# Optimization experiments

Hardware: AMD Instinct MI355X
Metric: run time of the kernel (lower is better)

## Reference

```python
import jax, jax.numpy as jnp
import numpy as np

TEMPERATURE = 0.5
COS_EPS = 1e-8  # torch.nn.CosineSimilarity default eps


def setup_inputs() -> dict:
    key = jax.random.key(0)
    k1, k2 = jax.random.split(key)
    N, D = 4096, 128
    z_i = jax.random.normal(k1, (N, D), dtype=jnp.float32)
    z_j = jax.random.normal(k2, (N, D), dtype=jnp.float32)
    return {"z_i": z_i, "z_j": z_j}


def reference(z_i, z_j):
    t = TEMPERATURE
    # L2-normalize each row (torch.norm over dim=1, then divide)
    zi = z_i / jnp.linalg.norm(z_i, axis=1, keepdims=True)
    zj = z_j / jnp.linalg.norm(z_j, axis=1, keepdims=True)
    z_ij = jnp.concatenate([zi, zj], axis=0)  # [2N, D]
    z_ji = jnp.concatenate([zj, zi], axis=0)  # [2N, D]
    # Full pairwise similarity matrix, scaled by temperature: [2N, 2N]
    sim = jnp.matmul(z_ij, z_ij.T) / t
    exp_sim = jnp.exp(sim)
    exp_sum = jnp.sum(exp_sim, axis=1)          # row reduction
    diag = jnp.diagonal(exp_sim)                # self-similarity terms
    # numerator: exp(cosine_similarity(z_ij, z_ji) / t) — positive pairs
    cos = jnp.sum(z_ij * z_ji, axis=1) / jnp.maximum(
        jnp.linalg.norm(z_ij, axis=1) * jnp.linalg.norm(z_ji, axis=1), COS_EPS)
    numerator = jnp.exp(cos / t)
    denominator = exp_sum - diag
    loss = -jnp.log(numerator / denominator)
    return jnp.mean(loss)
```

## Files before the change

### kernel.cpp

```cpp
#include <hip/hip_runtime.h>
#include <hip/hip_bf16.h>

typedef __attribute__((ext_vector_type(4))) int int4v;
typedef __attribute__((ext_vector_type(8))) int int8v;
typedef __attribute__((ext_vector_type(16))) float floatx16;

#define D_DIM 128
#define SCALE_F 1.6986436f
#define CS 16
#define CTILE 64
#define BLK_ROWS 256
#define MREP 2
#define UNIT_SCALE 0x7F7F7F7F

typedef __attribute__((address_space(1))) const unsigned int GUI;
typedef __attribute__((address_space(3))) unsigned int LUI;
#define GLOAD16(g, l) __builtin_amdgcn_global_load_lds((GUI*)(g), (LUI*)(l), 16, 0, 0)

__global__ void prep_kernel(const float* __restrict__ zi,
                            const float* __restrict__ zj,
                            unsigned char* __restrict__ Z8,
                            float* __restrict__ posdot,
                            float* __restrict__ selfarg, int N) {
    int r = blockIdx.x * 4 + (threadIdx.x >> 6);
    int t = threadIdx.x & 63;
    const float* pi = zi + (size_t)r * D_DIM;
    const float* pj = zj + (size_t)r * D_DIM;
    float a0 = pi[2 * t], a1 = pi[2 * t + 1];
    float b0 = pj[2 * t], b1 = pj[2 * t + 1];
    float ssi = a0*a0 + a1*a1;
    float ssj = b0*b0 + b1*b1;
    float sij = a0*b0 + a1*b1;
#pragma unroll
    for (int off = 1; off < 64; off <<= 1) {
        ssi += __shfl_xor(ssi, off);
        ssj += __shfl_xor(ssj, off);
        sij += __shfl_xor(sij, off);
    }
    float ni = sqrtf(ssi), nj = sqrtf(ssj);
    float ri = SCALE_F / ni, rj = SCALE_F / nj;
    int ui = __builtin_amdgcn_cvt_pk_fp8_f32(a0 * ri, a1 * ri, 0, false);
    int uj = __builtin_amdgcn_cvt_pk_fp8_f32(b0 * rj, b1 * rj, 0, false);
    *(ushort*)&Z8[(size_t)r * D_DIM + 2 * t]       = (ushort)(ui & 0xffff);
    *(ushort*)&Z8[(size_t)(r + N) * D_DIM + 2 * t] = (ushort)(uj & 0xffff);
    float fi0 = __builtin_amdgcn_cvt_f32_fp8(ui, 0);
    float fi1 = __builtin_amdgcn_cvt_f32_fp8(ui, 1);
    float fj0 = __builtin_amdgcn_cvt_f32_fp8(uj, 0);
    float fj1 = __builtin_amdgcn_cvt_f32_fp8(uj, 1);
    float sdi = fi0*fi0 + fi1*fi1;
    float sdj = fj0*fj0 + fj1*fj1;
#pragma unroll
    for (int off = 1; off < 64; off <<= 1) {
        sdi += __shfl_xor(sdi, off);
        sdj += __shfl_xor(sdj, off);
    }
    if (t == 0) {
        posdot[r] = sij / fmaxf(ni * nj, 1e-8f);
        selfarg[r]     = sdi;
        selfarg[r + N] = sdj;
    }
}

__global__ __launch_bounds__(512, 4)
void main_kernel(const unsigned char* __restrict__ Z8,
                 float* __restrict__ rowpart, int N2) {
    __shared__ unsigned char Btile[2][CTILE * D_DIM];

    const int tid  = threadIdx.x;
    const int lane = tid & 63;
    const int wave = tid >> 6;
    const int mw   = wave & 3;
    const int nh   = wave >> 2;
    const int c32  = lane & 31;
    const int h    = lane >> 5;
    const int rwave0 = blockIdx.x * BLK_ROWS + mw * 64;
    const int c0base = blockIdx.y * (N2 / CS);

    const int ntile = (N2 / CS) / CTILE;

    const int scol = tid >> 3;
    const int ssl  = (tid & 7) ^ (scol & 7);
    const unsigned char* gsrc = Z8 + (size_t)(c0base + scol) * D_DIM + ssl * 16;
    const size_t tadv = (size_t)CTILE * D_DIM;

    GLOAD16(gsrc, &Btile[0][(size_t)tid * 16]);

    int8v afrag[MREP][2];
#pragma unroll
    for (int rb = 0; rb < MREP; ++rb) {
        const unsigned char* ap = Z8 + (size_t)(rwave0 + rb * 32 + c32) * D_DIM + h * 32;
        afrag[rb][0] = *(const int8v*)(ap);
        afrag[rb][1] = *(const int8v*)(ap + 64);
    }
#pragma unroll
    for (int rb = 0; rb < MREP; ++rb) {
        asm volatile("" : "+v"(afrag[rb][0]));
        asm volatile("" : "+v"(afrag[rb][1]));
    }

    floatx16 rowacc[MREP];
#pragma unroll
    for (int rb = 0; rb < MREP; ++rb)
        rowacc[rb] = (floatx16)0.0f;

    __syncthreads();

    for (int t = 0; t < ntile; ++t) {
        if (t + 1 < ntile)
            GLOAD16(gsrc + (size_t)(t + 1) * tadv,
                    &Btile[(t + 1) & 1][(size_t)tid * 16]);

        const unsigned char* buf = Btile[t & 1];
        const int bcol = nh * 32 + c32;
        const int cb   = bcol * D_DIM;
        const int c7   = bcol & 7;
        int4v l00 = *(const int4v*)&buf[cb + (((h * 2 + 0) ^ c7) * 16)];
        int4v l01 = *(const int4v*)&buf[cb + (((h * 2 + 1) ^ c7) * 16)];
        int4v l10 = *(const int4v*)&buf[cb + (((4 + h * 2 + 0) ^ c7) * 16)];
        int4v l11 = *(const int4v*)&buf[cb + (((4 + h * 2 + 1) ^ c7) * 16)];
        int8v b0 = {l00[0], l00[1], l00[2], l00[3], l01[0], l01[1], l01[2], l01[3]};
        int8v b1 = {l10[0], l10[1], l10[2], l10[3], l11[0], l11[1], l11[2], l11[3]};

#pragma unroll
        for (int rb = 0; rb < MREP; ++rb) {
            floatx16 acc = (floatx16)0.0f;
            acc = __builtin_amdgcn_mfma_scale_f32_32x32x64_f8f6f4(
                      afrag[rb][0], b0, acc, 0, 0, 0, UNIT_SCALE, 0, UNIT_SCALE);
            acc = __builtin_amdgcn_mfma_scale_f32_32x32x64_f8f6f4(
                      afrag[rb][1], b1, acc, 0, 0, 0, UNIT_SCALE, 0, UNIT_SCALE);
#pragma unroll
            for (int g = 0; g < 16; ++g)
                rowacc[rb][g] += __builtin_amdgcn_exp2f(acc[g]);
        }
        __syncthreads();
    }

#pragma unroll
    for (int rb = 0; rb < MREP; ++rb)
#pragma unroll
        for (int g = 0; g < 16; ++g) {
            float v = rowacc[rb][g];
            v += __shfl_xor(v, 1);
            v += __shfl_xor(v, 2);
            v += __shfl_xor(v, 4);
            v += __shfl_xor(v, 8);
            v += __shfl_xor(v, 16);
            if (c32 == 0) {
                int grow = rwave0 + rb * 32 + (g & 3) + 8 * (g >> 2) + 4 * h;
                rowpart[(size_t)(blockIdx.y * 2 + nh) * N2 + grow] = v;
            }
        }
}

__global__ void finalize1_kernel(const float* __restrict__ rowpart,
                                 const float* __restrict__ selfarg,
                                 const float* __restrict__ posdot,
                                 float* __restrict__ bpart, int N2, int NP) {
    __shared__ float red[4];
    int tid = threadIdx.x;
    int r = blockIdx.x * 256 + tid;
    float d0 = 0.f, d1 = 0.f, d2 = 0.f, d3 = 0.f;
#pragma unroll
    for (int q = 0; q < 2 * CS; q += 4) {
        d0 += rowpart[(size_t)(q + 0) * N2 + r];
        d1 += rowpart[(size_t)(q + 1) * N2 + r];
        d2 += rowpart[(size_t)(q + 2) * N2 + r];
        d3 += rowpart[(size_t)(q + 3) * N2 + r];
    }
    float denom = (d0 + d1) + (d2 + d3);
    denom -= __builtin_amdgcn_exp2f(selfarg[r]);
    float pos = posdot[r < NP ? r : r - NP];
    float v = logf(denom) - 2.0f * pos;
#pragma unroll
    for (int off = 1; off < 64; off <<= 1) v += __shfl_xor(v, off);
    if ((tid & 63) == 0) red[tid >> 6] = v;
    __syncthreads();
    if (tid == 0) bpart[blockIdx.x] = red[0] + red[1] + red[2] + red[3];
}

__global__ void finalize2_kernel(const float* __restrict__ bpart,
                                 float* __restrict__ out, int nb, int N2) {
    int t = threadIdx.x;
    float v = (t < nb) ? bpart[t] : 0.0f;
#pragma unroll
    for (int off = 1; off < 64; off <<= 1) v += __shfl_xor(v, off);
    if (t == 0) out[0] = v / (float)N2;
}

extern "C" void kernel_launch(void* const* d_in, const int* in_sizes, int n_in,
                              void* d_out, int out_size, void* d_ws, size_t ws_size,
                              hipStream_t stream) {
    const float* zi = (const float*)d_in[0];
    const float* zj = (const float*)d_in[1];
    const int N  = in_sizes[0] / D_DIM;
    const int N2 = 2 * N;

    char* w = (char*)d_ws;
    unsigned char* Z8 = (unsigned char*)w;
    size_t off = (size_t)N2 * D_DIM;
    float* posdot  = (float*)(w + off);  off += (size_t)N  * sizeof(float);
    float* selfarg = (float*)(w + off);  off += (size_t)N2 * sizeof(float);
    float* rowpart = (float*)(w + off);  off += (size_t)(2 * CS) * N2 * sizeof(float);
    float* bpart   = (float*)(w + off);

    prep_kernel<<<N / 4, 256, 0, stream>>>(zi, zj, Z8, posdot, selfarg, N);
    dim3 grid(N2 / BLK_ROWS, CS);
    main_kernel<<<grid, 512, 0, stream>>>(Z8, rowpart, N2);
    const int nb = N2 / 256;
    finalize1_kernel<<<nb, 256, 0, stream>>>(rowpart, selfarg, posdot, bpart, N2, N);
    finalize2_kernel<<<1, 64, 0, stream>>>(bpart, (float*)d_out, nb, N2);
}
```

Before: 32.55 us.

## Fuse finalize kernels into main kernel via last-block atomic ticket

Removes the two finalize kernel launches. Each main_kernel block now increments a global ticket counter, and the last block to finish reduces all row partials and writes the mean loss. The ticket is reset inside prep_kernel. This saves two launch gaps, but the final reduction over 8192 rows x 32 partials now runs serially in a single 512-thread block, which may cost more than the launches it replaces.

```diff
diff --git a/kernel.cpp b/kernel.cpp
--- a/kernel.cpp
+++ b/kernel.cpp
@@ -12,6 +12,7 @@
 #define BLK_ROWS 256
 #define MREP 2
 #define UNIT_SCALE 0x7F7F7F7F
+#define NBLOCKS (32 * CS)
 
 typedef __attribute__((address_space(1))) const unsigned int GUI;
 typedef __attribute__((address_space(3))) unsigned int LUI;
@@ -21,7 +22,9 @@
                             const float* __restrict__ zj,
                             unsigned char* __restrict__ Z8,
                             float* __restrict__ posdot,
-                            float* __restrict__ selfarg, int N) {
+                            float* __restrict__ selfarg,
+                            int* __restrict__ ticket, int N) {
+    if (blockIdx.x == 0 && threadIdx.x == 0) *ticket = 0;
     int r = blockIdx.x * 4 + (threadIdx.x >> 6);
     int t = threadIdx.x & 63;
     const float* pi = zi + (size_t)r * D_DIM;
@@ -63,8 +66,14 @@
 
 __global__ __launch_bounds__(512, 4)
 void main_kernel(const unsigned char* __restrict__ Z8,
-                 float* __restrict__ rowpart, int N2) {
+                 float* __restrict__ rowpart,
+                 const float* __restrict__ selfarg,
+                 const float* __restrict__ posdot,
+                 int* __restrict__ ticket,
+                 float* __restrict__ out, int N2, int NP) {
     __shared__ unsigned char Btile[2][CTILE * D_DIM];
+    __shared__ float red[8];
+    __shared__ int lastFlag;
 
     const int tid  = threadIdx.x;
     const int lane = tid & 63;
@@ -150,41 +159,40 @@
                 rowpart[(size_t)(blockIdx.y * 2 + nh) * N2 + grow] = v;
             }
         }
-}
-
-__global__ void finalize1_kernel(const float* __restrict__ rowpart,
-                                 const float* __restrict__ selfarg,
-                                 const float* __restrict__ posdot,
-                                 float* __restrict__ bpart, int N2, int NP) {
-    __shared__ float red[4];
-    int tid = threadIdx.x;
-    int r = blockIdx.x * 256 + tid;
-    float d0 = 0.f, d1 = 0.f, d2 = 0.f, d3 = 0.f;
-#pragma unroll
-    for (int q = 0; q < 2 * CS; q += 4) {
-        d0 += rowpart[(size_t)(q + 0) * N2 + r];
-        d1 += rowpart[(size_t)(q + 1) * N2 + r];
-        d2 += rowpart[(size_t)(q + 2) * N2 + r];
-        d3 += rowpart[(size_t)(q + 3) * N2 + r];
-    }
-    float denom = (d0 + d1) + (d2 + d3);
-    denom -= __builtin_amdgcn_exp2f(selfarg[r]);
-    float pos = posdot[r < NP ? r : r - NP];
-    float v = logf(denom) - 2.0f * pos;
-#pragma unroll
-    for (int off = 1; off < 64; off <<= 1) v += __shfl_xor(v, off);
-    if ((tid & 63) == 0) red[tid >> 6] = v;
+
+    __threadfence();
+    if (tid == 0) {
+        int old = atomicAdd(ticket, 1);
+        lastFlag = (old == NBLOCKS - 1);
+    }
     __syncthreads();
-    if (tid == 0) bpart[blockIdx.x] = red[0] + red[1] + red[2] + red[3];
-}
-
-__global__ void finalize2_kernel(const float* __restrict__ bpart,
-                                 float* __restrict__ out, int nb, int N2) {
-    int t = threadIdx.x;
-    float v = (t < nb) ? bpart[t] : 0.0f;
-#pragma unroll
-    for (int off = 1; off < 64; off <<= 1) v += __shfl_xor(v, off);
-    if (t == 0) out[0] = v / (float)N2;
+    if (!lastFlag) return;
+    __threadfence();
+
+    float bsum = 0.0f;
+    for (int r = tid; r < N2; r += 512) {
+        float d0 = 0.f, d1 = 0.f, d2 = 0.f, d3 = 0.f;
+#pragma unroll 2
+        for (int p = 0; p < 2 * CS; p += 8) {
+            d0 += rowpart[(size_t)(p + 0) * N2 + r] + rowpart[(size_t)(p + 4) * N2 + r];
+            d1 += rowpart[(size_t)(p + 1) * N2 + r] + rowpart[(size_t)(p + 5) * N2 + r];
+            d2 += rowpart[(size_t)(p + 2) * N2 + r] + rowpart[(size_t)(p + 6) * N2 + r];
+            d3 += rowpart[(size_t)(p + 3) * N2 + r] + rowpart[(size_t)(p + 7) * N2 + r];
+        }
+        float denom = (d0 + d1) + (d2 + d3) - __builtin_amdgcn_exp2f(selfarg[r]);
+        float pos = posdot[r < NP ? r : r - NP];
+        bsum += logf(denom) - 2.0f * pos;
+    }
+#pragma unroll
+    for (int off = 1; off < 64; off <<= 1) bsum += __shfl_xor(bsum, off);
+    if (lane == 0) red[wave] = bsum;
+    __syncthreads();
+    if (tid == 0) {
+        float s = 0.0f;
+#pragma unroll
+        for (int wv = 0; wv < 8; ++wv) s += red[wv];
+        out[0] = s / (float)N2;
+    }
 }
 
 extern "C" void kernel_launch(void* const* d_in, const int* in_sizes, int n_in,
@@ -201,12 +209,10 @@
     float* posdot  = (float*)(w + off);  off += (size_t)N  * sizeof(float);
     float* selfarg = (float*)(w + off);  off += (size_t)N2 * sizeof(float);
     float* rowpart = (float*)(w + off);  off += (size_t)(2 * CS) * N2 * sizeof(float);
-    float* bpart   = (float*)(w + off);
-
-    prep_kernel<<<N / 4, 256, 0, stream>>>(zi, zj, Z8, posdot, selfarg, N);
+    int*   ticket  = (int*)(w + off);
+
+    prep_kernel<<<N / 4, 256, 0, stream>>>(zi, zj, Z8, posdot, selfarg, ticket, N);
     dim3 grid(N2 / BLK_ROWS, CS);
-    main_kernel<<<grid, 512, 0, stream>>>(Z8, rowpart, N2);
-    const int nb = N2 / 256;
-    finalize1_kernel<<<nb, 256, 0, stream>>>(rowpart, selfarg, posdot, bpart, N2, N);
-    finalize2_kernel<<<1, 64, 0, stream>>>(bpart, (float*)d_out, nb, N2);
+    main_kernel<<<grid, 512, 0, stream>>>(Z8, rowpart, selfarg, posdot, ticket,
+                                          (float*)d_out, N2, N);
 }
```

New measurement: 121.7 us. 274% more time.
